# Performance work log

Hardware: AMD Instinct MI355X
Metric: run time of the kernel (lower is better)

The kernel has to match this reference:

```python
import jax, jax.numpy as jnp
import numpy as np

N, D = 16384, 256

def setup_inputs() -> dict:
    key = jax.random.key(0)
    k1, k2 = jax.random.split(key)
    image_features = jax.random.normal(k1, (N, D), dtype=jnp.float32)
    text_features = jax.random.normal(k2, (N, D), dtype=jnp.float32)
    logit_scale = jnp.float32(14.285714)  # exp(log(1/0.07)), typical CLIP temperature
    targets = jnp.arange(N, dtype=jnp.int64)
    return {"image_features": image_features, "text_features": text_features,
            "logit_scale": logit_scale, "targets": targets}

def _cross_entropy(logits, targets):
    # mean over rows of -log_softmax(logits)[i, targets[i]]
    logp = jax.nn.log_softmax(logits, axis=-1)
    return -jnp.mean(jnp.take_along_axis(logp, targets[:, None], axis=-1))

def reference(image_features, text_features, logit_scale, targets):
    logits = logit_scale * (image_features @ text_features.T)  # [N, N]
    image_loss = _cross_entropy(logits, targets)
    text_loss = _cross_entropy(logits.T, targets)
    return (image_loss + text_loss) / 2.0
```

## Files before the change

### kernel.cpp

```cpp
#include <hip/hip_runtime.h>

#define N_ 16384
#define D_ 256
#define LOG2E 1.4426950408889634f
#define HEXP2(x) __builtin_amdgcn_exp2f(x)

typedef __attribute__((ext_vector_type(8))) short short8;
typedef __attribute__((ext_vector_type(16))) float floatx16;

typedef __attribute__((address_space(1))) const unsigned int gu32_t;
typedef __attribute__((address_space(3))) unsigned int lu32_t;

__device__ __forceinline__ void async16(const void* g, void* l) {
  __builtin_amdgcn_global_load_lds((gu32_t*)g, (lu32_t*)l, 16, 0, 0);
}

__device__ __forceinline__ unsigned short f2bf(float x) {
  unsigned int u = __float_as_uint(x);
  u += 0x7fffu + ((u >> 16) & 1u);
  return (unsigned short)(u >> 16);
}

__global__ void prep_pack(const float* __restrict__ img, const float* __restrict__ txt,
                          const float* __restrict__ ls, short* __restrict__ PA,
                          short* __restrict__ PB, float* __restrict__ diag2,
                          float* __restrict__ out) {
  const int tid = threadIdx.x;
  const int t = blockIdx.x * 1024 + tid;
  const int m = tid & 31, h = (tid >> 5) & 1, ks = (tid >> 6) & 15;
  const int G = blockIdx.x;
  const int row = G * 32 + m, col = ks * 16 + h * 8;
  const float s2 = ls[0] * LOG2E;
  const float4* sa = (const float4*)(img + (size_t)row * D_ + col);
  const float4* sb = (const float4*)(txt + (size_t)row * D_ + col);
  float4 a0 = sa[0], a1 = sa[1];
  float4 b0 = sb[0], b1 = sb[1];
  short8 oa, ob;
  oa[0] = (short)f2bf(a0.x * s2); oa[1] = (short)f2bf(a0.y * s2);
  oa[2] = (short)f2bf(a0.z * s2); oa[3] = (short)f2bf(a0.w * s2);
  oa[4] = (short)f2bf(a1.x * s2); oa[5] = (short)f2bf(a1.y * s2);
  oa[6] = (short)f2bf(a1.z * s2); oa[7] = (short)f2bf(a1.w * s2);
  ob[0] = (short)f2bf(b0.x); ob[1] = (short)f2bf(b0.y);
  ob[2] = (short)f2bf(b0.z); ob[3] = (short)f2bf(b0.w);
  ob[4] = (short)f2bf(b1.x); ob[5] = (short)f2bf(b1.y);
  ob[6] = (short)f2bf(b1.z); ob[7] = (short)f2bf(b1.w);
  ((short8*)PA)[t] = oa;
  ((short8*)PB)[t] = ob;

  float d = a0.x * b0.x + a0.y * b0.y + a0.z * b0.z + a0.w * b0.w
          + a1.x * b1.x + a1.y * b1.y + a1.z * b1.z + a1.w * b1.w;
  __shared__ float red[32][33];
  red[tid >> 5][m] = d;
  __syncthreads();
  if (tid < 32) {
    float s = 0.f;
    #pragma unroll
    for (int q = 0; q < 32; ++q) s += red[q][tid];
    diag2[G * 32 + tid] = s * s2;
  }
  if (t == 0) out[0] = 0.f;
}

__global__ __launch_bounds__(256, 2)
void gemm_stats(const short* __restrict__ PA, const short* __restrict__ PB,
                float2* __restrict__ pR, float2* __restrict__ pC) {
  __shared__ __align__(16) char smem[73728];
  float* rowbuf  = (float*)(smem + 32768);
  float2* colbuf = (float2*)(smem + 71680);

  const int tid = threadIdx.x, lane = tid & 63, wv = tid >> 6;
  const int wr = wv >> 1, wc = wv & 1;
  const int m = lane & 31, h = lane >> 5;
  const int stripe = blockIdx.x, by = blockIdx.y;

  short8 areg[2][16];
  #pragma unroll
  for (int g = 0; g < 2; ++g)
    #pragma unroll
    for (int ks = 0; ks < 16; ++ks)
      areg[g][ks] = *(const short8*)(PA +
          ((size_t)((stripe * 4 + wr * 2 + g) * 16 + ks)) * 512 + lane * 8);
  asm volatile("s_waitcnt vmcnt(0)" ::: "memory");

  floatx16 acc[2][2];

  auto issue = [&](int jj2, int c2, int bufsel) {
    const short* base = PB + ((size_t)((by * 64 + jj2 * 4) * 16) + c2 * 4 + wv) * 512 + lane * 8;
    char* dst = smem + bufsel * 16384 + wv * 1024;
    #pragma unroll
    for (int ct = 0; ct < 4; ++ct)
      async16(base + (size_t)ct * 8192, dst + ct * 4096);
  };
  auto compute = [&](int c, int bufsel) {
    char* base = smem + bufsel * 16384 + lane * 16;
    #pragma unroll
    for (int ksl = 0; ksl < 4; ++ksl) {
      short8 b0 = *(const short8*)(base + ((wc * 2 + 0) * 4 + ksl) * 1024);
      short8 b1 = *(const short8*)(base + ((wc * 2 + 1) * 4 + ksl) * 1024);
      int ks = c * 4 + ksl;
      acc[0][0] = __builtin_amdgcn_mfma_f32_32x32x16_bf16(areg[0][ks], b0, acc[0][0], 0, 0, 0);
      acc[1][0] = __builtin_amdgcn_mfma_f32_32x32x16_bf16(areg[1][ks], b0, acc[1][0], 0, 0, 0);
      acc[0][1] = __builtin_amdgcn_mfma_f32_32x32x16_bf16(areg[0][ks], b1, acc[0][1], 0, 0, 0);
      acc[1][1] = __builtin_amdgcn_mfma_f32_32x32x16_bf16(areg[1][ks], b1, acc[1][1], 0, 0, 0);
    }
  };

  issue(0, 0, 0);
  issue(0, 1, 1);

  float Mr = -3.0e38f, Sr = 0.f;

  for (int jj = 0; jj < 16; ++jj) {
    #pragma unroll
    for (int rt = 0; rt < 2; ++rt)
      #pragma unroll
      for (int ctl = 0; ctl < 2; ++ctl)
        #pragma unroll
        for (int r = 0; r < 16; ++r) acc[rt][ctl][r] = 0.f;

    #pragma unroll
    for (int c = 0; c < 4; ++c) {
      if (jj == 15 && c == 3) { asm volatile("s_waitcnt vmcnt(0)" ::: "memory"); }
      else                    { asm volatile("s_waitcnt vmcnt(4)" ::: "memory"); }
      __builtin_amdgcn_s_barrier();
      asm volatile("" ::: "memory");
      compute(c, c & 1);
      asm volatile("" ::: "memory");
      __builtin_amdgcn_s_barrier();
      asm volatile("" ::: "memory");
      int nc = c + 2;
      int jj2 = jj + (nc >> 2);
      if (jj2 < 16) issue(jj2, nc & 3, nc & 1);
    }

    float vm[4];
    #pragma unroll
    for (int q = 0; q < 4; ++q) {
      float a01 = fmaxf(acc[q >> 1][q & 1][0],  acc[q >> 1][q & 1][1]);
      float a23 = fmaxf(acc[q >> 1][q & 1][2],  acc[q >> 1][q & 1][3]);
      float a45 = fmaxf(acc[q >> 1][q & 1][4],  acc[q >> 1][q & 1][5]);
      float a67 = fmaxf(acc[q >> 1][q & 1][6],  acc[q >> 1][q & 1][7]);
      float a89 = fmaxf(acc[q >> 1][q & 1][8],  acc[q >> 1][q & 1][9]);
      float aab = fmaxf(acc[q >> 1][q & 1][10], acc[q >> 1][q & 1][11]);
      float acd = fmaxf(acc[q >> 1][q & 1][12], acc[q >> 1][q & 1][13]);
      float aef = fmaxf(acc[q >> 1][q & 1][14], acc[q >> 1][q & 1][15]);
      vm[q] = fmaxf(fmaxf(fmaxf(a01, a23), fmaxf(a45, a67)),
                    fmaxf(fmaxf(a89, aab), fmaxf(acd, aef)));
    }
    float v = fmaxf(fmaxf(vm[0], vm[1]), fmaxf(vm[2], vm[3]));
    #pragma unroll
    for (int off = 1; off < 64; off <<= 1) v = fmaxf(v, __shfl_xor(v, off));
    float msub = v - 96.f;

    #pragma unroll
    for (int rt = 0; rt < 2; ++rt)
      #pragma unroll
      for (int ctl = 0; ctl < 2; ++ctl)
        #pragma unroll
        for (int r = 0; r < 16; ++r) acc[rt][ctl][r] = HEXP2(acc[rt][ctl][r] - msub);

    #pragma unroll
    for (int ctl = 0; ctl < 2; ++ctl) {
      float cp = 0.f;
      #pragma unroll
      for (int r = 0; r < 16; ++r) cp += acc[0][ctl][r] + acc[1][ctl][r];
      cp += __shfl_xor(cp, 32);
      if (h == 0) colbuf[wr * 128 + wc * 64 + ctl * 32 + m] = make_float2(msub, cp);
    }

    #pragma unroll
    for (int rt = 0; rt < 2; ++rt)
      #pragma unroll
      for (int rq = 0; rq < 4; ++rq) {
        float4 rp;
        rp.x = acc[rt][0][rq * 4 + 0] + acc[rt][1][rq * 4 + 0];
        rp.y = acc[rt][0][rq * 4 + 1] + acc[rt][1][rq * 4 + 1];
        rp.z = acc[rt][0][rq * 4 + 2] + acc[rt][1][rq * 4 + 2];
        rp.w = acc[rt][0][rq * 4 + 3] + acc[rt][1][rq * 4 + 3];
        *(float4*)&rowbuf[(wr * 64 + wc * 32 + m) * 76 + rt * 32 + rq * 8 + h * 4] = rp;
      }
    asm volatile("s_waitcnt lgkmcnt(0)" ::: "memory");
    __builtin_amdgcn_s_barrier();
    asm volatile("" ::: "memory");

    {
      float s = 0.f;
      #pragma unroll
      for (int k = 0; k < 32; ++k)
        s += rowbuf[(wr * 64 + h * 32 + k) * 76 + wc * 32 + m];
      s += __shfl_xor(s, 32);
      if (s > 0.f) {
        if (msub > Mr) { Sr = Sr * HEXP2(Mr - msub) + s; Mr = msub; }
        else           { Sr += s * HEXP2(msub - Mr); }
      }
    }
    if (tid < 128) {
      float2 c0 = colbuf[tid], c1 = colbuf[128 + tid];
      float M = -3.0e38f, L = 0.f;
      if (c0.y > 0.f) { M = c0.x; L = c0.y; }
      if (c1.y > 0.f) {
        if (c1.x > M) { L = L * HEXP2(M - c1.x) + c1.y; M = c1.x; }
        else          { L += c1.y * HEXP2(c1.x - M); }
      }
      pC[(size_t)stripe * N_ + by * 2048 + jj * 128 + tid] = make_float2(M, L);
    }
    asm volatile("s_waitcnt lgkmcnt(0)" ::: "memory");
    __builtin_amdgcn_s_barrier();
    asm volatile("" ::: "memory");
  }

  if (h == 0)
    pR[(size_t)by * N_ + stripe * 128 + wr * 64 + wc * 32 + m] = make_float2(Mr, Sr);
}

__global__ void merge_kernel(const float2* __restrict__ pR, const float2* __restrict__ pC,
                             const float* __restrict__ diag2, float* __restrict__ out) {
  auto mrg = [](float& M, float& L, float2 w) {
    if (w.y > 0.f) {
      if (w.x > M) { L = L * exp2f(M - w.x) + w.y; M = w.x; }
      else         { L += w.y * exp2f(w.x - M); }
    }
  };
  const int b = blockIdx.x, tid = threadIdx.x;
  float val = 0.f;

  if (b < 64) {
    int i = b * 256 + tid;
    float M = -3.0e38f, L = 0.f;
    #pragma unroll
    for (int g = 0; g < 8; ++g) mrg(M, L, pR[(size_t)g * N_ + i]);
    val = (M + log2f(fmaxf(L, 1e-45f))) - diag2[i];
  } else {
    int cb = b - 64;
    int i = cb * 32 + (tid & 31);
    int s0 = (tid >> 5) * 16;
    float M = -3.0e38f, L = 0.f;
    #pragma unroll
    for (int k = 0; k < 16; ++k) mrg(M, L, pC[(size_t)(s0 + k) * N_ + i]);
    __shared__ float2 part[8][32];
    part[tid >> 5][tid & 31] = make_float2(M, L);
    __syncthreads();
    if (tid < 32) {
      float M2 = -3.0e38f, L2 = 0.f;
      #pragma unroll
      for (int q = 0; q < 8; ++q) mrg(M2, L2, part[q][tid]);
      val = (M2 + log2f(fmaxf(L2, 1e-45f))) - diag2[cb * 32 + tid];
    }
  }

  __shared__ float red[256];
  red[tid] = val;
  __syncthreads();
  #pragma unroll
  for (int s = 128; s > 0; s >>= 1) {
    if (tid < s) red[tid] += red[tid + s];
    __syncthreads();
  }
  if (tid == 0)
    atomicAdd(out, red[0] * (0.69314718055994531f / 32768.0f));
}

extern "C" void kernel_launch(void* const* d_in, const int* in_sizes, int n_in,
                              void* d_out, int out_size, void* d_ws, size_t ws_size,
                              hipStream_t stream) {
  const float* img = (const float*)d_in[0];
  const float* txt = (const float*)d_in[1];
  const float* ls  = (const float*)d_in[2];
  float* out = (float*)d_out;

  char* ws = (char*)d_ws;
  short* PA    = (short*)(ws);
  short* PB    = (short*)(ws + 8388608);
  float* diag2 = (float*)(ws + 16777216);
  float2* pR   = (float2*)(ws + 16843008);
  float2* pC   = (float2*)(ws + 17891584);

  hipLaunchKernelGGL(prep_pack, dim3(512), dim3(1024), 0, stream, img, txt, ls, PA, PB, diag2, out);
  hipLaunchKernelGGL(gemm_stats, dim3(128, 8), dim3(256), 0, stream, PA, PB, pR, pC);
  hipLaunchKernelGGL(merge_kernel, dim3(576), dim3(256), 0, stream, pR, pC, diag2, out);
}
```

Before: 242.2 us.

## Pre-reduce row sums with lane shuffles to shrink LDS and raise occupancy

Row partial sums of the exponentiated tile are now first reduced across lanes with xor shuffles, so each wave writes a much smaller row buffer to LDS, and the final per-row sum reads four float4 values instead of 32 strided scalars. The smaller buffer cuts shared memory per block from 72 KB to 44 KB, and launch bounds go from 2 to 3 blocks per CU to use the freed space. The cost is 64 extra cross-lane shuffles per tile and predicated scalar LDS stores. The tighter launch bound may also force register spills, since the kernel keeps a large A fragment and accumulators in registers.

```diff
diff --git a/kernel.cpp b/kernel.cpp
--- a/kernel.cpp
+++ b/kernel.cpp
@@ -61,12 +61,12 @@
   if (t == 0) out[0] = 0.f;
 }
 
-__global__ __launch_bounds__(256, 2)
+__global__ __launch_bounds__(256, 3)
 void gemm_stats(const short* __restrict__ PA, const short* __restrict__ PB,
                 float2* __restrict__ pR, float2* __restrict__ pC) {
-  __shared__ __align__(16) char smem[73728];
-  float* rowbuf  = (float*)(smem + 32768);
-  float2* colbuf = (float2*)(smem + 71680);
+  __shared__ __align__(16) char smem[45056];
+  float* rowbuf2 = (float*)(smem + 32768);
+  float2* colbuf = (float2*)(smem + 43008);
 
   const int tid = threadIdx.x, lane = tid & 63, wv = tid >> 6;
   const int wr = wv >> 1, wc = wv & 1;
@@ -168,27 +168,36 @@
       if (h == 0) colbuf[wr * 128 + wc * 64 + ctl * 32 + m] = make_float2(msub, cp);
     }
 
-    #pragma unroll
-    for (int rt = 0; rt < 2; ++rt)
-      #pragma unroll
-      for (int rq = 0; rq < 4; ++rq) {
-        float4 rp;
-        rp.x = acc[rt][0][rq * 4 + 0] + acc[rt][1][rq * 4 + 0];
-        rp.y = acc[rt][0][rq * 4 + 1] + acc[rt][1][rq * 4 + 1];
-        rp.z = acc[rt][0][rq * 4 + 2] + acc[rt][1][rq * 4 + 2];
-        rp.w = acc[rt][0][rq * 4 + 3] + acc[rt][1][rq * 4 + 3];
-        *(float4*)&rowbuf[(wr * 64 + wc * 32 + m) * 76 + rt * 32 + rq * 8 + h * 4] = rp;
+    float rp[2][16];
+    #pragma unroll
+    for (int rt = 0; rt < 2; ++rt)
+      #pragma unroll
+      for (int r = 0; r < 16; ++r) {
+        float x = acc[rt][0][r] + acc[rt][1][r];
+        x += __shfl_xor(x, 8);
+        x += __shfl_xor(x, 16);
+        rp[rt][r] = x;
       }
+    #pragma unroll
+    for (int rt = 0; rt < 2; ++rt)
+      #pragma unroll
+      for (int r = 0; r < 16; ++r)
+        if ((m >> 3) == rt)
+          rowbuf2[(size_t)(wr * 64 + rt * 32 + (r & 3) + 8 * (r >> 2) + 4 * h) * 20 +
+                  wc * 8 + (m & 7)] = rp[rt][r];
+
     asm volatile("s_waitcnt lgkmcnt(0)" ::: "memory");
     __builtin_amdgcn_s_barrier();
     asm volatile("" ::: "memory");
 
     {
-      float s = 0.f;
-      #pragma unroll
-      for (int k = 0; k < 32; ++k)
-        s += rowbuf[(wr * 64 + h * 32 + k) * 76 + wc * 32 + m];
-      s += __shfl_xor(s, 32);
+      const float* rb = rowbuf2 + (size_t)(wr * 64 + wc * 32 + m) * 20;
+      float4 q0 = *(const float4*)(rb + 0);
+      float4 q1 = *(const float4*)(rb + 4);
+      float4 q2 = *(const float4*)(rb + 8);
+      float4 q3 = *(const float4*)(rb + 12);
+      float s = ((q0.x + q0.y) + (q0.z + q0.w)) + ((q1.x + q1.y) + (q1.z + q1.w))
+              + ((q2.x + q2.y) + (q2.z + q2.w)) + ((q3.x + q3.y) + (q3.z + q3.w));
       if (s > 0.f) {
         if (msub > Mr) { Sr = Sr * HEXP2(Mr - msub) + s; Mr = msub; }
         else           { Sr += s * HEXP2(msub - Mr); }
```

After: 424.3 us. +75.2%, slower.
